# Optimization experiments

Hardware: AMD Instinct MI355X
Metric: run time of the kernel (lower is better)

## Reference

```python
import jax, jax.numpy as jnp
import numpy as np

N_NODES = 100000


def _graph_conv_right(feat, src, dst, W, b, n_nodes):
    # DGL GraphConv(norm='right'): since in_feats > out_feats, apply weight first,
    # then sum-aggregate messages over edges, divide by in-degree (clamped >= 1),
    # add bias, then relu activation.
    h = feat @ W                                   # [N, out]
    msg = jnp.take(h, src, axis=0)                 # [E, out] gather from source nodes
    agg = jax.ops.segment_sum(msg, dst, num_segments=n_nodes)  # [N, out]
    deg = jax.ops.segment_sum(jnp.ones_like(dst, dtype=feat.dtype), dst,
                              num_segments=n_nodes)
    deg = jnp.clip(deg, 1.0, None)                 # allow_zero_in_degree
    out = agg / deg[:, None] + b
    return jax.nn.relu(out)


def setup_inputs() -> dict:
    key = jax.random.key(0)
    ks = jax.random.split(key, 6)
    n_edges = 3200000
    in_dim, hidden_dim, out_dim = 128, 32, 12
    features = jax.random.normal(ks[0], (N_NODES, in_dim), dtype=jnp.float32)
    src = jax.random.randint(ks[1], (n_edges,), 0, N_NODES, dtype=jnp.int64 if jax.config.jax_enable_x64 else jnp.int32)
    dst = jax.random.randint(ks[2], (n_edges,), 0, N_NODES, dtype=jnp.int64 if jax.config.jax_enable_x64 else jnp.int32)
    W1 = jax.random.normal(ks[3], (in_dim, hidden_dim), dtype=jnp.float32) * (1.0 / np.sqrt(in_dim))
    b1 = jnp.zeros((hidden_dim,), dtype=jnp.float32)
    W2 = jax.random.normal(ks[4], (hidden_dim, out_dim), dtype=jnp.float32) * (1.0 / np.sqrt(hidden_dim))
    b2 = jnp.zeros((out_dim,), dtype=jnp.float32)
    return {"features": features, "src": src, "dst": dst,
            "W1": W1, "b1": b1, "W2": W2, "b2": b2}


def reference(features, src, dst, W1, b1, W2, b2):
    x = _graph_conv_right(features, src, dst, W1, b1, N_NODES)
    x = jax.nn.relu(x)  # extra F.relu after layer1 (idempotent, kept for fidelity)
    x = _graph_conv_right(x, src, dst, W2, b2, N_NODES)
    return x
```

## Files before the change

kernel.cpp:

```cpp
#include <hip/hip_runtime.h>
#include <hip/hip_fp16.h>

#define N_IN   128
#define HID    32
#define ODIM   12
#define H2P    16
#define RNODES 64
#define RSH    6
#define NBMAX  1600
#define NBK2   2048
#define BCAP   2432
#define CHUNK  8192

__global__ __launch_bounds__(256) void gemm1_kernel(const float* __restrict__ feat,
                                                    const float* __restrict__ W1,
                                                    __half* __restrict__ h1,
                                                    int* __restrict__ bcur, int nNodes) {
    if (blockIdx.x == 0) {
        ((int4*)bcur)[threadIdx.x]       = make_int4(0, 0, 0, 0);
        ((int4*)bcur)[threadIdx.x + 256] = make_int4(0, 0, 0, 0);
    }
    __shared__ float sF[64 * 132];
    __shared__ float sW[N_IN * HID];
    const int tid = threadIdx.x;
    const int nb  = blockIdx.x * 64;

    {
        const float4* Wv  = (const float4*)W1;
        float4*       sWv = (float4*)sW;
        #pragma unroll
        for (int i = 0; i < 4; ++i) sWv[tid + 256 * i] = Wv[tid + 256 * i];
    }
    #pragma unroll
    for (int i = 0; i < 8; ++i) {
        int f   = tid + 256 * i;
        int row = f >> 5;
        int c4  = f & 31;
        int n   = nb + row;
        float4 v = make_float4(0.f, 0.f, 0.f, 0.f);
        if (n < nNodes) v = *(const float4*)(feat + (size_t)n * N_IN + c4 * 4);
        *(float4*)(sF + row * 132 + c4 * 4) = v;
    }
    __syncthreads();

    const int og = tid & 7;
    const int ng = tid >> 3;
    const int o0 = og * 4;
    const float* f0 = sF + ng * 132;
    const float* f1 = sF + (ng + 32) * 132;

    float acc0[4] = {0.f, 0.f, 0.f, 0.f};
    float acc1[4] = {0.f, 0.f, 0.f, 0.f};
    #pragma unroll 8
    for (int k = 0; k < N_IN; k += 4) {
        float4 a0 = *(const float4*)(f0 + k);
        float4 a1 = *(const float4*)(f1 + k);
        const float a0v[4] = {a0.x, a0.y, a0.z, a0.w};
        const float a1v[4] = {a1.x, a1.y, a1.z, a1.w};
        #pragma unroll
        for (int j = 0; j < 4; ++j) {
            float4 w = *(const float4*)(sW + (k + j) * HID + o0);
            acc0[0] += a0v[j] * w.x; acc0[1] += a0v[j] * w.y;
            acc0[2] += a0v[j] * w.z; acc0[3] += a0v[j] * w.w;
            acc1[0] += a1v[j] * w.x; acc1[1] += a1v[j] * w.y;
            acc1[2] += a1v[j] * w.z; acc1[3] += a1v[j] * w.w;
        }
    }
    int n0 = nb + ng, n1 = nb + ng + 32;
    if (n0 < nNodes) {
        union { __half2 h[2]; float2 f; } u;
        u.h[0] = __floats2half2_rn(acc0[0], acc0[1]);
        u.h[1] = __floats2half2_rn(acc0[2], acc0[3]);
        *(float2*)(h1 + (size_t)n0 * HID + o0) = u.f;
    }
    if (n1 < nNodes) {
        union { __half2 h[2]; float2 f; } u;
        u.h[0] = __floats2half2_rn(acc1[0], acc1[1]);
        u.h[1] = __floats2half2_rn(acc1[2], acc1[3]);
        *(float2*)(h1 + (size_t)n1 * HID + o0) = u.f;
    }
}

__global__ __launch_bounds__(512) void bplace_kernel(const int* __restrict__ src,
                                                     const int* __restrict__ dst,
                                                     int* __restrict__ bcur,
                                                     int* __restrict__ pairs, int nEdges) {
    __shared__ int      lh[NBK2];
    __shared__ int      lcur[NBK2];
    __shared__ int      gofs[NBK2];
    __shared__ int      sWS[16];
    __shared__ int      lst[CHUNK];
    __shared__ unsigned short lbk[CHUNK];

    const int tid  = threadIdx.x;
    const int base = blockIdx.x * CHUNK;
    const int m    = min(CHUNK, nEdges - base);

    ((int4*)lh)[tid] = make_int4(0, 0, 0, 0);
    __syncthreads();

    int4 dv[4], sv[4];
    bool ok[4];
    #pragma unroll
    for (int k = 0; k < 4; ++k) {
        int e = base + k * 2048 + tid * 4;
        ok[k] = (e < nEdges);
        if (ok[k]) {
            dv[k] = *(const int4*)(dst + e);
            sv[k] = *(const int4*)(src + e);
        }
    }
    #pragma unroll
    for (int k = 0; k < 4; ++k) {
        if (ok[k]) {
            atomicAdd(&lh[dv[k].x >> RSH], 1);
            atomicAdd(&lh[dv[k].y >> RSH], 1);
            atomicAdd(&lh[dv[k].z >> RSH], 1);
            atomicAdd(&lh[dv[k].w >> RSH], 1);
        }
    }
    __syncthreads();

    int4 cc = ((int4*)lh)[tid];
    int tsum = cc.x + cc.y + cc.z + cc.w;
    const int lane = tid & 63, wid = tid >> 6;
    int inc = tsum;
    #pragma unroll
    for (int off = 1; off < 64; off <<= 1) {
        int t = __shfl_up(inc, off, 64);
        if (lane >= off) inc += t;
    }
    if (lane == 63) sWS[wid] = inc;
    __syncthreads();
    if (tid == 0) {
        int r = 0;
        #pragma unroll
        for (int w = 0; w < 8; ++w) { int s = sWS[w]; sWS[8 + w] = r; r += s; }
    }
    __syncthreads();
    int excl = sWS[8 + wid] + inc - tsum;
    const int b0 = 4 * tid;
    int e0 = excl, e1 = e0 + cc.x, e2 = e1 + cc.y, e3 = e2 + cc.z;
    lh[b0]     = e0; lh[b0 + 1]   = e1; lh[b0 + 2]   = e2; lh[b0 + 3]   = e3;
    lcur[b0]   = e0; lcur[b0 + 1] = e1; lcur[b0 + 2] = e2; lcur[b0 + 3] = e3;
    gofs[b0]     = (cc.x > 0) ? atomicAdd(&bcur[b0],     cc.x) : 0;
    gofs[b0 + 1] = (cc.y > 0) ? atomicAdd(&bcur[b0 + 1], cc.y) : 0;
    gofs[b0 + 2] = (cc.z > 0) ? atomicAdd(&bcur[b0 + 2], cc.z) : 0;
    gofs[b0 + 3] = (cc.w > 0) ? atomicAdd(&bcur[b0 + 3], cc.w) : 0;
    __syncthreads();

    #pragma unroll
    for (int k = 0; k < 4; ++k) {
        if (ok[k]) {
            int b, p;
            b = dv[k].x >> RSH; p = atomicAdd(&lcur[b], 1); lst[p] = ((dv[k].x & (RNODES - 1)) << 17) | sv[k].x; lbk[p] = (unsigned short)b;
            b = dv[k].y >> RSH; p = atomicAdd(&lcur[b], 1); lst[p] = ((dv[k].y & (RNODES - 1)) << 17) | sv[k].y; lbk[p] = (unsigned short)b;
            b = dv[k].z >> RSH; p = atomicAdd(&lcur[b], 1); lst[p] = ((dv[k].z & (RNODES - 1)) << 17) | sv[k].z; lbk[p] = (unsigned short)b;
            b = dv[k].w >> RSH; p = atomicAdd(&lcur[b], 1); lst[p] = ((dv[k].w & (RNODES - 1)) << 17) | sv[k].w; lbk[p] = (unsigned short)b;
        }
    }
    __syncthreads();

    for (int i = tid; i < m; i += 512) {
        int b = lbk[i];
        int rank = gofs[b] + (i - lh[b]);
        if (rank < BCAP) pairs[(size_t)b * BCAP + rank] = lst[i];
    }
}

__global__ __launch_bounds__(512) void agg1_kernel(const __half* __restrict__ h1,
                                                   const int* __restrict__ bcur,
                                                   int* __restrict__ pairs,
                                                   const float* __restrict__ b1,
                                                   const float* __restrict__ W2,
                                                   __half* __restrict__ h2,
                                                   float* __restrict__ rdeg,
                                                   int* __restrict__ rowstartg,
                                                   int* __restrict__ countg, int nNodes) {
    __shared__ int   sorted[BCAP];
    __shared__ int   hist[RNODES];
    __shared__ int   scn[RNODES];
    __shared__ int   cur[RNODES];
    __shared__ float sW2[HID * ODIM];
    const int tid = threadIdx.x;
    const int bkt = blockIdx.x;
    const int cnt = min(bcur[bkt], BCAP);
    const size_t pb = (size_t)bkt * BCAP;

    if (tid < RNODES) hist[tid] = 0;
    if (tid < 96) ((float4*)sW2)[tid] = ((const float4*)W2)[tid];
    __syncthreads();

    for (int i = tid; i < cnt; i += 512) atomicAdd(&hist[pairs[pb + i] >> 17], 1);
    __syncthreads();

    if (tid < RNODES) {
        int v0 = hist[tid];
        int inc = v0;
        #pragma unroll
        for (int off = 1; off < RNODES; off <<= 1) {
            int t = __shfl_up(inc, off, 64);
            if (tid >= off) inc += t;
        }
        scn[tid] = inc - v0;
        cur[tid] = inc - v0;
    }
    __syncthreads();

    for (int i = tid; i < cnt; i += 512) {
        int v = pairs[pb + i];
        int pos = atomicAdd(&cur[v >> 17], 1);
        sorted[pos] = v & 0x1FFFF;
    }
    __syncthreads();

    for (int i = tid; i < cnt; i += 512) pairs[pb + i] = sorted[i];
    if (tid < RNODES) {
        int n = bkt * RNODES + tid;
        if (n < nNodes) {
            rowstartg[n] = (int)pb + scn[tid];
            countg[n]    = hist[tid];
        }
    }

    const int c   = tid & 15;
    const int grp = tid >> 4;
    const __half2* h1v = (const __half2*)h1;
    const int col = (c < ODIM) ? c : 0;

    #pragma unroll
    for (int g = 0; g < 2; ++g) {
        int nl = g * 32 + grp;
        int n  = bkt * RNODES + nl;
        if (n >= nNodes) continue;
        int dcnt = hist[nl];
        int beg  = scn[nl];
        int end  = beg + dcnt;

        float2 s0 = {0.f, 0.f}, s1 = {0.f, 0.f}, s2 = {0.f, 0.f}, s3 = {0.f, 0.f};
        int i = beg;
        for (; i + 8 <= end; i += 8) {
            int e0 = sorted[i],     e1 = sorted[i + 1], e2 = sorted[i + 2], e3 = sorted[i + 3];
            int e4 = sorted[i + 4], e5 = sorted[i + 5], e6 = sorted[i + 6], e7 = sorted[i + 7];
            float2 f0 = __half22float2(h1v[(size_t)e0 * 16 + c]);
            float2 f1 = __half22float2(h1v[(size_t)e1 * 16 + c]);
            float2 f2 = __half22float2(h1v[(size_t)e2 * 16 + c]);
            float2 f3 = __half22float2(h1v[(size_t)e3 * 16 + c]);
            float2 f4 = __half22float2(h1v[(size_t)e4 * 16 + c]);
            float2 f5 = __half22float2(h1v[(size_t)e5 * 16 + c]);
            float2 f6 = __half22float2(h1v[(size_t)e6 * 16 + c]);
            float2 f7 = __half22float2(h1v[(size_t)e7 * 16 + c]);
            s0.x += f0.x; s0.y += f0.y;  s1.x += f1.x; s1.y += f1.y;
            s2.x += f2.x; s2.y += f2.y;  s3.x += f3.x; s3.y += f3.y;
            s0.x += f4.x; s0.y += f4.y;  s1.x += f5.x; s1.y += f5.y;
            s2.x += f6.x; s2.y += f6.y;  s3.x += f7.x; s3.y += f7.y;
        }
        for (; i + 4 <= end; i += 4) {
            int e0 = sorted[i], e1 = sorted[i + 1], e2 = sorted[i + 2], e3 = sorted[i + 3];
            float2 f0 = __half22float2(h1v[(size_t)e0 * 16 + c]);
            float2 f1 = __half22float2(h1v[(size_t)e1 * 16 + c]);
            float2 f2 = __half22float2(h1v[(size_t)e2 * 16 + c]);
            float2 f3 = __half22float2(h1v[(size_t)e3 * 16 + c]);
            s0.x += f0.x; s0.y += f0.y;  s1.x += f1.x; s1.y += f1.y;
            s2.x += f2.x; s2.y += f2.y;  s3.x += f3.x; s3.y += f3.y;
        }
        for (; i < end; ++i) {
            float2 f = __half22float2(h1v[(size_t)sorted[i] * 16 + c]);
            s0.x += f.x; s0.y += f.y;
        }
        float sumx = (s0.x + s1.x) + (s2.x + s3.x);
        float sumy = (s0.y + s1.y) + (s2.y + s3.y);

        float rd = 1.f / (float)(dcnt < 1 ? 1 : dcnt);
        float x0 = sumx * rd + b1[2 * c];
        float x1 = sumy * rd + b1[2 * c + 1];
        x0 = x0 > 0.f ? x0 : 0.f;
        x1 = x1 > 0.f ? x1 : 0.f;

        float acc = 0.f;
        #pragma unroll
        for (int k = 0; k < 16; ++k) {
            float xk0 = __shfl(x0, k, 16);
            float xk1 = __shfl(x1, k, 16);
            acc += xk0 * sW2[(2 * k) * ODIM + col] + xk1 * sW2[(2 * k + 1) * ODIM + col];
        }
        if (c < ODIM) h2[(size_t)n * H2P + c] = __float2half(acc);
        if (c == 0)   rdeg[n] = rd;
    }
}

__global__ __launch_bounds__(256) void agg2_kernel(const __half* __restrict__ h2,
                                                   const int* __restrict__ rowstartg,
                                                   const int* __restrict__ countg,
                                                   const int* __restrict__ eidx,
                                                   const float* __restrict__ rdeg,
                                                   const float* __restrict__ b2,
                                                   float* __restrict__ out, int nNodes) {
    const int tid = threadIdx.x;
    const int n = blockIdx.x * 32 + (tid >> 3);
    const int c = tid & 7;
    if (n >= nNodes) return;

    const int cnt = countg[n];
    const int beg = rowstartg[n];
    const int end = beg + cnt;
    const int cc  = (c < 6) ? c : 0;
    const __half2* h2v = (const __half2*)h2;

    float2 s0 = {0.f, 0.f}, s1 = {0.f, 0.f}, s2 = {0.f, 0.f}, s3 = {0.f, 0.f};
    int i = beg;
    for (; i + 8 <= end; i += 8) {
        int e0 = eidx[i],     e1 = eidx[i + 1], e2 = eidx[i + 2], e3 = eidx[i + 3];
        int e4 = eidx[i + 4], e5 = eidx[i + 5], e6 = eidx[i + 6], e7 = eidx[i + 7];
        float2 f0 = __half22float2(h2v[(size_t)e0 * 8 + cc]);
        float2 f1 = __half22float2(h2v[(size_t)e1 * 8 + cc]);
        float2 f2 = __half22float2(h2v[(size_t)e2 * 8 + cc]);
        float2 f3 = __half22float2(h2v[(size_t)e3 * 8 + cc]);
        float2 f4 = __half22float2(h2v[(size_t)e4 * 8 + cc]);
        float2 f5 = __half22float2(h2v[(size_t)e5 * 8 + cc]);
        float2 f6 = __half22float2(h2v[(size_t)e6 * 8 + cc]);
        float2 f7 = __half22float2(h2v[(size_t)e7 * 8 + cc]);
        s0.x += f0.x; s0.y += f0.y;  s1.x += f1.x; s1.y += f1.y;
        s2.x += f2.x; s2.y += f2.y;  s3.x += f3.x; s3.y += f3.y;
        s0.x += f4.x; s0.y += f4.y;  s1.x += f5.x; s1.y += f5.y;
        s2.x += f6.x; s2.y += f6.y;  s3.x += f7.x; s3.y += f7.y;
    }
    for (; i + 4 <= end; i += 4) {
        int e0 = eidx[i], e1 = eidx[i + 1], e2 = eidx[i + 2], e3 = eidx[i + 3];
        float2 f0 = __half22float2(h2v[(size_t)e0 * 8 + cc]);
        float2 f1 = __half22float2(h2v[(size_t)e1 * 8 + cc]);
        float2 f2 = __half22float2(h2v[(size_t)e2 * 8 + cc]);
        float2 f3 = __half22float2(h2v[(size_t)e3 * 8 + cc]);
        s0.x += f0.x; s0.y += f0.y;  s1.x += f1.x; s1.y += f1.y;
        s2.x += f2.x; s2.y += f2.y;  s3.x += f3.x; s3.y += f3.y;
    }
    for (; i < end; ++i) {
        float2 f = __half22float2(h2v[(size_t)eidx[i] * 8 + cc]);
        s0.x += f.x; s0.y += f.y;
    }
    float sumx = (s0.x + s1.x) + (s2.x + s3.x);
    float sumy = (s0.y + s1.y) + (s2.y + s3.y);

    float rd = rdeg[n];
    float w0 = sumx * rd + b2[2 * cc];
    float w1 = sumy * rd + b2[2 * cc + 1];
    w0 = w0 > 0.f ? w0 : 0.f;
    w1 = w1 > 0.f ? w1 : 0.f;
    if (c < 6) *(float2*)(out + (size_t)n * ODIM + 2 * c) = make_float2(w0, w1);
}

extern "C" void kernel_launch(void* const* d_in, const int* in_sizes, int n_in,
                              void* d_out, int out_size, void* d_ws, size_t ws_size,
                              hipStream_t stream) {
    const float* feat = (const float*)d_in[0];
    const int*   src  = (const int*)d_in[1];
    const int*   dst  = (const int*)d_in[2];
    const float* W1   = (const float*)d_in[3];
    const float* b1   = (const float*)d_in[4];
    const float* W2   = (const float*)d_in[5];
    const float* b2   = (const float*)d_in[6];
    float* out = (float*)d_out;

    const int nEdges = in_sizes[1];
    const int nNodes = in_sizes[0] / N_IN;
    const int nb     = (nNodes + RNODES - 1) / RNODES;

    __half* h1       = (__half*)d_ws;
    __half* h2       = h1 + (size_t)nNodes * HID;
    float*  rdeg     = (float*)(h2 + (size_t)nNodes * H2P);
    int*    rowstart = (int*)(rdeg + nNodes);
    int*    countg   = rowstart + nNodes;
    int*    bcur     = countg + nNodes;
    int*    pairs    = bcur + NBK2;

    gemm1_kernel<<<(nNodes + 63) / 64, 256, 0, stream>>>(feat, W1, h1, bcur, nNodes);
    bplace_kernel<<<(nEdges + CHUNK - 1) / CHUNK, 512, 0, stream>>>(src, dst, bcur, pairs, nEdges);
    agg1_kernel<<<nb, 512, 0, stream>>>(h1, bcur, pairs, b1, W2, h2, rdeg, rowstart, countg, nNodes);
    agg2_kernel<<<(nNodes + 31) / 32, 256, 0, stream>>>(h2, rowstart, countg, pairs, rdeg, b2, out, nNodes);
}
```

Measured before the change: 231.7 us.

## Simplify edge bucketing and widen gathers to 16-byte loads in both aggregations

The bucket placement kernel drops the in-block scan and shared staging. It now handles 2048 edges per block and writes each edge straight to global memory at a slot reserved with shared and global atomics. Both aggregation kernels switch from half2 gathers to float4 gathers: 8 threads per node, each loading a quarter of a row, with several edges accumulated in parallel and combined by shuffle reductions. Layer-2 output is written with float4 stores from one or two lanes. Global writes become scattered and uncoalesced, and 4x more blocks contend on the bucket counters.

```diff
diff --git a/kernel.cpp b/kernel.cpp
--- a/kernel.cpp
+++ b/kernel.cpp
@@ -10,7 +10,19 @@
 #define NBMAX  1600
 #define NBK2   2048
 #define BCAP   2432
-#define CHUNK  8192
+#define CHUNK  2048
+
+__device__ __forceinline__ void acc_f4(float (&acc)[8], float4 vf) {
+    union { float4 f; __half2 h[4]; } uu; uu.f = vf;
+    float2 g0 = __half22float2(uu.h[0]);
+    float2 g1 = __half22float2(uu.h[1]);
+    float2 g2 = __half22float2(uu.h[2]);
+    float2 g3 = __half22float2(uu.h[3]);
+    acc[0] += g0.x; acc[1] += g0.y;
+    acc[2] += g1.x; acc[3] += g1.y;
+    acc[4] += g2.x; acc[5] += g2.y;
+    acc[6] += g3.x; acc[7] += g3.y;
+}
 
 __global__ __launch_bounds__(256) void gemm1_kernel(const float* __restrict__ feat,
                                                     const float* __restrict__ W1,
@@ -85,86 +97,48 @@
                                                      const int* __restrict__ dst,
                                                      int* __restrict__ bcur,
                                                      int* __restrict__ pairs, int nEdges) {
-    __shared__ int      lh[NBK2];
-    __shared__ int      lcur[NBK2];
-    __shared__ int      gofs[NBK2];
-    __shared__ int      sWS[16];
-    __shared__ int      lst[CHUNK];
-    __shared__ unsigned short lbk[CHUNK];
+    __shared__ int lh[NBK2];
+    __shared__ int lcur[NBK2];
 
     const int tid  = threadIdx.x;
     const int base = blockIdx.x * CHUNK;
-    const int m    = min(CHUNK, nEdges - base);
 
     ((int4*)lh)[tid] = make_int4(0, 0, 0, 0);
     __syncthreads();
 
-    int4 dv[4], sv[4];
-    bool ok[4];
-    #pragma unroll
-    for (int k = 0; k < 4; ++k) {
-        int e = base + k * 2048 + tid * 4;
-        ok[k] = (e < nEdges);
-        if (ok[k]) {
-            dv[k] = *(const int4*)(dst + e);
-            sv[k] = *(const int4*)(src + e);
-        }
-    }
-    #pragma unroll
-    for (int k = 0; k < 4; ++k) {
-        if (ok[k]) {
-            atomicAdd(&lh[dv[k].x >> RSH], 1);
-            atomicAdd(&lh[dv[k].y >> RSH], 1);
-            atomicAdd(&lh[dv[k].z >> RSH], 1);
-            atomicAdd(&lh[dv[k].w >> RSH], 1);
-        }
-    }
-    __syncthreads();
-
-    int4 cc = ((int4*)lh)[tid];
-    int tsum = cc.x + cc.y + cc.z + cc.w;
-    const int lane = tid & 63, wid = tid >> 6;
-    int inc = tsum;
-    #pragma unroll
-    for (int off = 1; off < 64; off <<= 1) {
-        int t = __shfl_up(inc, off, 64);
-        if (lane >= off) inc += t;
-    }
-    if (lane == 63) sWS[wid] = inc;
-    __syncthreads();
-    if (tid == 0) {
-        int r = 0;
-        #pragma unroll
-        for (int w = 0; w < 8; ++w) { int s = sWS[w]; sWS[8 + w] = r; r += s; }
-    }
-    __syncthreads();
-    int excl = sWS[8 + wid] + inc - tsum;
-    const int b0 = 4 * tid;
-    int e0 = excl, e1 = e0 + cc.x, e2 = e1 + cc.y, e3 = e2 + cc.z;
-    lh[b0]     = e0; lh[b0 + 1]   = e1; lh[b0 + 2]   = e2; lh[b0 + 3]   = e3;
-    lcur[b0]   = e0; lcur[b0 + 1] = e1; lcur[b0 + 2] = e2; lcur[b0 + 3] = e3;
-    gofs[b0]     = (cc.x > 0) ? atomicAdd(&bcur[b0],     cc.x) : 0;
-    gofs[b0 + 1] = (cc.y > 0) ? atomicAdd(&bcur[b0 + 1], cc.y) : 0;
-    gofs[b0 + 2] = (cc.z > 0) ? atomicAdd(&bcur[b0 + 2], cc.z) : 0;
-    gofs[b0 + 3] = (cc.w > 0) ? atomicAdd(&bcur[b0 + 3], cc.w) : 0;
-    __syncthreads();
-
-    #pragma unroll
-    for (int k = 0; k < 4; ++k) {
-        if (ok[k]) {
-            int b, p;
-            b = dv[k].x >> RSH; p = atomicAdd(&lcur[b], 1); lst[p] = ((dv[k].x & (RNODES - 1)) << 17) | sv[k].x; lbk[p] = (unsigned short)b;
-            b = dv[k].y >> RSH; p = atomicAdd(&lcur[b], 1); lst[p] = ((dv[k].y & (RNODES - 1)) << 17) | sv[k].y; lbk[p] = (unsigned short)b;
-            b = dv[k].z >> RSH; p = atomicAdd(&lcur[b], 1); lst[p] = ((dv[k].z & (RNODES - 1)) << 17) | sv[k].z; lbk[p] = (unsigned short)b;
-            b = dv[k].w >> RSH; p = atomicAdd(&lcur[b], 1); lst[p] = ((dv[k].w & (RNODES - 1)) << 17) | sv[k].w; lbk[p] = (unsigned short)b;
-        }
-    }
-    __syncthreads();
-
-    for (int i = tid; i < m; i += 512) {
-        int b = lbk[i];
-        int rank = gofs[b] + (i - lh[b]);
-        if (rank < BCAP) pairs[(size_t)b * BCAP + rank] = lst[i];
+    const int e = base + tid * 4;
+    const bool ok = (e < nEdges);
+    int4 dv, sv;
+    if (ok) {
+        dv = *(const int4*)(dst + e);
+        sv = *(const int4*)(src + e);
+        atomicAdd(&lh[dv.x >> RSH], 1);
+        atomicAdd(&lh[dv.y >> RSH], 1);
+        atomicAdd(&lh[dv.z >> RSH], 1);
+        atomicAdd(&lh[dv.w >> RSH], 1);
+    }
+    __syncthreads();
+
+    {
+        const int b0 = 4 * tid;
+        int4 c = ((int4*)lh)[tid];
+        if (c.x > 0) lcur[b0]     = atomicAdd(&bcur[b0],     c.x);
+        if (c.y > 0) lcur[b0 + 1] = atomicAdd(&bcur[b0 + 1], c.y);
+        if (c.z > 0) lcur[b0 + 2] = atomicAdd(&bcur[b0 + 2], c.z);
+        if (c.w > 0) lcur[b0 + 3] = atomicAdd(&bcur[b0 + 3], c.w);
+    }
+    __syncthreads();
+
+    if (ok) {
+        int b, r;
+        b = dv.x >> RSH; r = atomicAdd(&lcur[b], 1);
+        if (r < BCAP) pairs[(size_t)b * BCAP + r] = ((dv.x & (RNODES - 1)) << 17) | sv.x;
+        b = dv.y >> RSH; r = atomicAdd(&lcur[b], 1);
+        if (r < BCAP) pairs[(size_t)b * BCAP + r] = ((dv.y & (RNODES - 1)) << 17) | sv.y;
+        b = dv.z >> RSH; r = atomicAdd(&lcur[b], 1);
+        if (r < BCAP) pairs[(size_t)b * BCAP + r] = ((dv.z & (RNODES - 1)) << 17) | sv.z;
+        b = dv.w >> RSH; r = atomicAdd(&lcur[b], 1);
+        if (r < BCAP) pairs[(size_t)b * BCAP + r] = ((dv.w & (RNODES - 1)) << 17) | sv.w;
     }
 }
 
@@ -223,73 +197,70 @@
         }
     }
 
-    const int c   = tid & 15;
-    const int grp = tid >> 4;
-    const __half2* h1v = (const __half2*)h1;
-    const int col = (c < ODIM) ? c : 0;
-
-    #pragma unroll
-    for (int g = 0; g < 2; ++g) {
-        int nl = g * 32 + grp;
-        int n  = bkt * RNODES + nl;
-        if (n >= nNodes) continue;
-        int dcnt = hist[nl];
-        int beg  = scn[nl];
-        int end  = beg + dcnt;
-
-        float2 s0 = {0.f, 0.f}, s1 = {0.f, 0.f}, s2 = {0.f, 0.f}, s3 = {0.f, 0.f};
+    const int r   = tid & 7;
+    const int grp = tid >> 3;
+    const int q   = r & 3;
+    const int sub = r >> 2;
+    const float4* h1q = (const float4*)h1;
+    const int n = bkt * RNODES + grp;
+
+    if (n < nNodes) {
+        const int dcnt = hist[grp];
+        const int beg  = scn[grp];
+        const int end  = beg + dcnt;
+
+        float acc[8] = {0.f, 0.f, 0.f, 0.f, 0.f, 0.f, 0.f, 0.f};
         int i = beg;
-        for (; i + 8 <= end; i += 8) {
-            int e0 = sorted[i],     e1 = sorted[i + 1], e2 = sorted[i + 2], e3 = sorted[i + 3];
-            int e4 = sorted[i + 4], e5 = sorted[i + 5], e6 = sorted[i + 6], e7 = sorted[i + 7];
-            float2 f0 = __half22float2(h1v[(size_t)e0 * 16 + c]);
-            float2 f1 = __half22float2(h1v[(size_t)e1 * 16 + c]);
-            float2 f2 = __half22float2(h1v[(size_t)e2 * 16 + c]);
-            float2 f3 = __half22float2(h1v[(size_t)e3 * 16 + c]);
-            float2 f4 = __half22float2(h1v[(size_t)e4 * 16 + c]);
-            float2 f5 = __half22float2(h1v[(size_t)e5 * 16 + c]);
-            float2 f6 = __half22float2(h1v[(size_t)e6 * 16 + c]);
-            float2 f7 = __half22float2(h1v[(size_t)e7 * 16 + c]);
-            s0.x += f0.x; s0.y += f0.y;  s1.x += f1.x; s1.y += f1.y;
-            s2.x += f2.x; s2.y += f2.y;  s3.x += f3.x; s3.y += f3.y;
-            s0.x += f4.x; s0.y += f4.y;  s1.x += f5.x; s1.y += f5.y;
-            s2.x += f6.x; s2.y += f6.y;  s3.x += f7.x; s3.y += f7.y;
-        }
-        for (; i + 4 <= end; i += 4) {
-            int e0 = sorted[i], e1 = sorted[i + 1], e2 = sorted[i + 2], e3 = sorted[i + 3];
-            float2 f0 = __half22float2(h1v[(size_t)e0 * 16 + c]);
-            float2 f1 = __half22float2(h1v[(size_t)e1 * 16 + c]);
-            float2 f2 = __half22float2(h1v[(size_t)e2 * 16 + c]);
-            float2 f3 = __half22float2(h1v[(size_t)e3 * 16 + c]);
-            s0.x += f0.x; s0.y += f0.y;  s1.x += f1.x; s1.y += f1.y;
-            s2.x += f2.x; s2.y += f2.y;  s3.x += f3.x; s3.y += f3.y;
-        }
-        for (; i < end; ++i) {
-            float2 f = __half22float2(h1v[(size_t)sorted[i] * 16 + c]);
-            s0.x += f.x; s0.y += f.y;
-        }
-        float sumx = (s0.x + s1.x) + (s2.x + s3.x);
-        float sumy = (s0.y + s1.y) + (s2.y + s3.y);
-
-        float rd = 1.f / (float)(dcnt < 1 ? 1 : dcnt);
-        float x0 = sumx * rd + b1[2 * c];
-        float x1 = sumy * rd + b1[2 * c + 1];
-        x0 = x0 > 0.f ? x0 : 0.f;
-        x1 = x1 > 0.f ? x1 : 0.f;
-
-        float acc = 0.f;
-        #pragma unroll
-        for (int k = 0; k < 16; ++k) {
-            float xk0 = __shfl(x0, k, 16);
-            float xk1 = __shfl(x1, k, 16);
-            acc += xk0 * sW2[(2 * k) * ODIM + col] + xk1 * sW2[(2 * k + 1) * ODIM + col];
-        }
-        if (c < ODIM) h2[(size_t)n * H2P + c] = __float2half(acc);
-        if (c == 0)   rdeg[n] = rd;
-    }
-}
-
-__global__ __launch_bounds__(256) void agg2_kernel(const __half* __restrict__ h2,
+        for (; i + 16 <= end; i += 16) {
+            float4 v[8];
+            #pragma unroll
+            for (int u = 0; u < 8; ++u) {
+                int e = sorted[i + 2 * u + sub];
+                v[u] = h1q[(size_t)e * 4 + q];
+            }
+            #pragma unroll
+            for (int u = 0; u < 8; ++u) acc_f4(acc, v[u]);
+        }
+        for (; i + 2 <= end; i += 2) {
+            int e = sorted[i + sub];
+            acc_f4(acc, h1q[(size_t)e * 4 + q]);
+        }
+        if (i < end && sub == 0) {
+            int e = sorted[i];
+            acc_f4(acc, h1q[(size_t)e * 4 + q]);
+        }
+
+        #pragma unroll
+        for (int t = 0; t < 8; ++t) acc[t] += __shfl_xor(acc[t], 4, 8);
+
+        const float rd = 1.f / (float)(dcnt < 1 ? 1 : dcnt);
+        float x[8];
+        #pragma unroll
+        for (int t = 0; t < 8; ++t) {
+            float xv = acc[t] * rd + b1[8 * q + t];
+            x[t] = xv > 0.f ? xv : 0.f;
+        }
+
+        const int j0  = r;
+        const int j1m = (r < 4) ? (r + 8) : r;
+        float o0 = 0.f, o1 = 0.f;
+        #pragma unroll
+        for (int qq = 0; qq < 4; ++qq) {
+            #pragma unroll
+            for (int t = 0; t < 8; ++t) {
+                float xv = __shfl(x[t], qq, 8);
+                int k = 8 * qq + t;
+                o0 += xv * sW2[k * ODIM + j0];
+                o1 += xv * sW2[k * ODIM + j1m];
+            }
+        }
+        h2[(size_t)n * H2P + j0] = __float2half(o0);
+        if (r < 4) h2[(size_t)n * H2P + 8 + r] = __float2half(o1);
+        if (r == 0) rdeg[n] = rd;
+    }
+}
+
+__global__ __launch_bounds__(512) void agg2_kernel(const __half* __restrict__ h2,
                                                    const int* __restrict__ rowstartg,
                                                    const int* __restrict__ countg,
                                                    const int* __restrict__ eidx,
@@ -297,56 +268,66 @@
                                                    const float* __restrict__ b2,
                                                    float* __restrict__ out, int nNodes) {
     const int tid = threadIdx.x;
-    const int n = blockIdx.x * 32 + (tid >> 3);
-    const int c = tid & 7;
+    const int grp = tid >> 3;
+    const int r   = tid & 7;
+    const int n   = blockIdx.x * 64 + grp;
     if (n >= nNodes) return;
+
+    const int half = r & 1;
+    const int sub  = r >> 1;
+    const float4* h2q = (const float4*)h2;
 
     const int cnt = countg[n];
     const int beg = rowstartg[n];
     const int end = beg + cnt;
-    const int cc  = (c < 6) ? c : 0;
-    const __half2* h2v = (const __half2*)h2;
-
-    float2 s0 = {0.f, 0.f}, s1 = {0.f, 0.f}, s2 = {0.f, 0.f}, s3 = {0.f, 0.f};
+
+    float acc[8] = {0.f, 0.f, 0.f, 0.f, 0.f, 0.f, 0.f, 0.f};
     int i = beg;
-    for (; i + 8 <= end; i += 8) {
-        int e0 = eidx[i],     e1 = eidx[i + 1], e2 = eidx[i + 2], e3 = eidx[i + 3];
-        int e4 = eidx[i + 4], e5 = eidx[i + 5], e6 = eidx[i + 6], e7 = eidx[i + 7];
-        float2 f0 = __half22float2(h2v[(size_t)e0 * 8 + cc]);
-        float2 f1 = __half22float2(h2v[(size_t)e1 * 8 + cc]);
-        float2 f2 = __half22float2(h2v[(size_t)e2 * 8 + cc]);
-        float2 f3 = __half22float2(h2v[(size_t)e3 * 8 + cc]);
-        float2 f4 = __half22float2(h2v[(size_t)e4 * 8 + cc]);
-        float2 f5 = __half22float2(h2v[(size_t)e5 * 8 + cc]);
-        float2 f6 = __half22float2(h2v[(size_t)e6 * 8 + cc]);
-        float2 f7 = __half22float2(h2v[(size_t)e7 * 8 + cc]);
-        s0.x += f0.x; s0.y += f0.y;  s1.x += f1.x; s1.y += f1.y;
-        s2.x += f2.x; s2.y += f2.y;  s3.x += f3.x; s3.y += f3.y;
-        s0.x += f4.x; s0.y += f4.y;  s1.x += f5.x; s1.y += f5.y;
-        s2.x += f6.x; s2.y += f6.y;  s3.x += f7.x; s3.y += f7.y;
+    for (; i + 32 <= end; i += 32) {
+        float4 v[8];
+        #pragma unroll
+        for (int u = 0; u < 8; ++u) {
+            int e = eidx[i + 4 * u + sub];
+            v[u] = h2q[(size_t)e * 2 + half];
+        }
+        #pragma unroll
+        for (int u = 0; u < 8; ++u) acc_f4(acc, v[u]);
     }
     for (; i + 4 <= end; i += 4) {
-        int e0 = eidx[i], e1 = eidx[i + 1], e2 = eidx[i + 2], e3 = eidx[i + 3];
-        float2 f0 = __half22float2(h2v[(size_t)e0 * 8 + cc]);
-        float2 f1 = __half22float2(h2v[(size_t)e1 * 8 + cc]);
-        float2 f2 = __half22float2(h2v[(size_t)e2 * 8 + cc]);
-        float2 f3 = __half22float2(h2v[(size_t)e3 * 8 + cc]);
-        s0.x += f0.x; s0.y += f0.y;  s1.x += f1.x; s1.y += f1.y;
-        s2.x += f2.x; s2.y += f2.y;  s3.x += f3.x; s3.y += f3.y;
-    }
-    for (; i < end; ++i) {
-        float2 f = __half22float2(h2v[(size_t)eidx[i] * 8 + cc]);
-        s0.x += f.x; s0.y += f.y;
-    }
-    float sumx = (s0.x + s1.x) + (s2.x + s3.x);
-    float sumy = (s0.y + s1.y) + (s2.y + s3.y);
-
-    float rd = rdeg[n];
-    float w0 = sumx * rd + b2[2 * cc];
-    float w1 = sumy * rd + b2[2 * cc + 1];
-    w0 = w0 > 0.f ? w0 : 0.f;
-    w1 = w1 > 0.f ? w1 : 0.f;
-    if (c < 6) *(float2*)(out + (size_t)n * ODIM + 2 * c) = make_float2(w0, w1);
+        int e = eidx[i + sub];
+        acc_f4(acc, h2q[(size_t)e * 2 + half]);
+    }
+    const int rem = end - i;
+    if (sub < rem) {
+        int e = eidx[i + sub];
+        acc_f4(acc, h2q[(size_t)e * 2 + half]);
+    }
+
+    #pragma unroll
+    for (int t = 0; t < 8; ++t) {
+        acc[t] += __shfl_xor(acc[t], 2, 8);
+        acc[t] += __shfl_xor(acc[t], 4, 8);
+    }
+
+    const float rd = rdeg[n];
+    if (r == 0) {
+        float w[8];
+        #pragma unroll
+        for (int t = 0; t < 8; ++t) {
+            float wv = acc[t] * rd + b2[t];
+            w[t] = wv > 0.f ? wv : 0.f;
+        }
+        *(float4*)(out + (size_t)n * ODIM)     = make_float4(w[0], w[1], w[2], w[3]);
+        *(float4*)(out + (size_t)n * ODIM + 4) = make_float4(w[4], w[5], w[6], w[7]);
+    } else if (r == 1) {
+        float w[4];
+        #pragma unroll
+        for (int t = 0; t < 4; ++t) {
+            float wv = acc[t] * rd + b2[8 + t];
+            w[t] = wv > 0.f ? wv : 0.f;
+        }
+        *(float4*)(out + (size_t)n * ODIM + 8) = make_float4(w[0], w[1], w[2], w[3]);
+    }
 }
 
 extern "C" void kernel_launch(void* const* d_in, const int* in_sizes, int n_in,
@@ -376,5 +357,5 @@
     gemm1_kernel<<<(nNodes + 63) / 64, 256, 0, stream>>>(feat, W1, h1, bcur, nNodes);
     bplace_kernel<<<(nEdges + CHUNK - 1) / CHUNK, 512, 0, stream>>>(src, dst, bcur, pairs, nEdges);
     agg1_kernel<<<nb, 512, 0, stream>>>(h1, bcur, pairs, b1, W2, h2, rdeg, rowstart, countg, nNodes);
-    agg2_kernel<<<(nNodes + 31) / 32, 256, 0, stream>>>(h2, rowstart, countg, pairs, rdeg, b2, out, nNodes);
-}
+    agg2_kernel<<<(nNodes + 63) / 64, 512, 0, stream>>>(h2, rowstart, countg, pairs, rdeg, b2, out, nNodes);
+}
```

Result: slower. 340.6 us (+47.0%).
